# Optimization experiments

Measured on AMD Instinct MI355X. Metric: run time of the kernel, lower is better.

The kernel has to match this reference:

```python
import jax, jax.numpy as jnp
import numpy as np

NUM_GROUPS = 8
NUM_HEADS = 4
EPS = 1e-5


def group_norm(x, w, b):
    # x: [B, C, H, W]; normalize over (C/G, H, W) within each of G groups
    B, C, H, W = x.shape
    xg = x.reshape(B, NUM_GROUPS, C // NUM_GROUPS, H, W)
    mean = xg.mean(axis=(2, 3, 4), keepdims=True)
    var = xg.var(axis=(2, 3, 4), keepdims=True)
    xn = ((xg - mean) * jax.lax.rsqrt(var + EPS)).reshape(B, C, H, W)
    return xn * w[None, :, None, None] + b[None, :, None, None]


def setup_inputs() -> dict:
    key = jax.random.key(0)
    ks = jax.random.split(key, 7)
    B, C, H, W = 4, 256, 64, 64
    x = jax.random.normal(ks[0], (B, C, H, W), dtype=jnp.float32)
    gn_w = jax.random.normal(ks[1], (C,), dtype=jnp.float32) * 0.1 + 1.0
    gn_b = jax.random.normal(ks[2], (C,), dtype=jnp.float32) * 0.1
    qkv_w = jax.random.normal(ks[3], (3 * C, C), dtype=jnp.float32) / np.sqrt(C)
    qkv_b = jax.random.normal(ks[4], (3 * C,), dtype=jnp.float32) * 0.02
    proj_w = jax.random.normal(ks[5], (C, C), dtype=jnp.float32) / np.sqrt(C)
    proj_b = jax.random.normal(ks[6], (C,), dtype=jnp.float32) * 0.02
    return {"x": x, "gn_w": gn_w, "gn_b": gn_b, "qkv_w": qkv_w,
            "qkv_b": qkv_b, "proj_w": proj_w, "proj_b": proj_b}


def reference(x, gn_w, gn_b, qkv_w, qkv_b, proj_w, proj_b):
    B, C, H, W = x.shape
    nh = NUM_HEADS
    hd = C // nh
    scale = hd ** -0.5
    N = H * W

    h = group_norm(x, gn_w, gn_b)
    # 1x1 conv == channel matmul: [B, 3C, H, W]
    qkv = jnp.einsum('oc,bchw->bohw', qkv_w, h) + qkv_b[None, :, None, None]
    qkv = qkv.reshape(B, 3, nh, hd, N)  # matches torch .view(B,3,nh,hd,HW)
    q, k, v = qkv[:, 0], qkv[:, 1], qkv[:, 2]  # each [B, nh, hd, N]

    attn = jnp.einsum('bhdn,bhdm->bhnm', q, k) * scale  # [B, nh, N, N]
    attn = jax.nn.softmax(attn, axis=-1)
    out = jnp.einsum('bhnm,bhdm->bhdn', attn, v)  # [B, nh, hd, N]
    out = out.reshape(B, C, H, W)

    proj = jnp.einsum('oc,bchw->bohw', proj_w, out) + proj_b[None, :, None, None]
    return x + proj
```

## Files before the change

### kernel.cpp

```cpp
#include <hip/hip_runtime.h>
#include <hip/hip_bf16.h>

#define BB   4
#define CC   256
#define NN   4096
#define NH   4
#define HD   64
#define NG   8
#define GSZ  32
#define EPSV 1e-5f
#define SCALE_L2E 0.18033688f

typedef __bf16 bf16x8 __attribute__((ext_vector_type(8)));
typedef float  f32x4  __attribute__((ext_vector_type(4)));
typedef short  short4v __attribute__((ext_vector_type(4)));

#define MFMA16(a, b, c)  __builtin_amdgcn_mfma_f32_16x16x32_bf16((a), (b), (c), 0, 0, 0)
#define MFMAPV(a, b, c)  __builtin_amdgcn_mfma_f32_16x16x16bf16_1k((a), (b), (c), 0, 0, 0)

#if __has_builtin(__builtin_amdgcn_exp2f)
#define EXP2F __builtin_amdgcn_exp2f
#else
#define EXP2F exp2f
#endif

__device__ inline unsigned short f2bf(float f) {
    unsigned int u = __float_as_uint(f);
    u += 0x7fffu + ((u >> 16) & 1u);
    return (unsigned short)(u >> 16);
}

__device__ __forceinline__ short4v pk4(float p0, float p1, float p2, float p3) {
    alignas(8) unsigned int u[2];
    u[0] = __builtin_amdgcn_perm(__float_as_uint(p1) + 0x8000u,
                                 __float_as_uint(p0) + 0x8000u, 0x07060302u);
    u[1] = __builtin_amdgcn_perm(__float_as_uint(p3) + 0x8000u,
                                 __float_as_uint(p2) + 0x8000u, 0x07060302u);
    return *reinterpret_cast<short4v*>(u);
}

__device__ __forceinline__ void async_ld16(void* lds, const void* g) {
    __builtin_amdgcn_global_load_lds(
        (const __attribute__((address_space(1))) unsigned int*)g,
        (__attribute__((address_space(3))) unsigned int*)lds, 16, 0, 0);
}

__global__ void k_prep(const float* __restrict__ x, float* __restrict__ stats,
                       const float* __restrict__ wq, const float* __restrict__ wp,
                       unsigned short* __restrict__ oq, unsigned short* __restrict__ op) {
    int blk = blockIdx.x;
    int t = threadIdx.x;
    if (blk >= 256) {
        int i = (blk - 256) * 256 + t;
        if (i < 3 * CC * CC) oq[i] = f2bf(wq[i]);
        if (i < CC * CC)     op[i] = f2bf(wp[i]);
        return;
    }
    int b = blk >> 6, g = (blk >> 3) & 7, s = blk & 7;
    const float* p = x + ((size_t)(b * CC + g * GSZ)) * NN + s * 16384;
    float s0 = 0.f, s1 = 0.f;
    #pragma unroll
    for (int i = 0; i < 64; ++i) { float v = p[i * 256 + t]; s0 += v; s1 += v * v; }
    #pragma unroll
    for (int m = 1; m <= 32; m <<= 1) { s0 += __shfl_xor(s0, m); s1 += __shfl_xor(s1, m); }
    __shared__ float ls[8];
    int w = t >> 6;
    if ((t & 63) == 0) { ls[w * 2] = s0; ls[w * 2 + 1] = s1; }
    __syncthreads();
    if (t == 0) {
        float a0 = ls[0] + ls[2] + ls[4] + ls[6];
        float a1 = ls[1] + ls[3] + ls[5] + ls[7];
        atomicAdd(&stats[(b * NG + g) * 2 + 0], a0);
        atomicAdd(&stats[(b * NG + g) * 2 + 1], a1);
    }
}

__global__ void k_gnapply(const float* __restrict__ x, const float* __restrict__ gw,
                          const float* __restrict__ gb, const float* __restrict__ stats,
                          unsigned short* __restrict__ ht) {
    int b = blockIdx.z, ct = blockIdx.y, nt = blockIdx.x;
    int c0 = ct * 32, n0 = nt * 64;
    int t = threadIdx.x;
    __shared__ float tile[32][65];
    const float* xp = x + ((size_t)(b * CC + c0)) * NN + n0;
    int cl = t >> 6, nl = t & 63;
    #pragma unroll
    for (int p = 0; p < 8; ++p)
        tile[p * 4 + cl][nl] = xp[(size_t)(p * 4 + cl) * NN + nl];
    float sum = stats[(b * NG + ct) * 2 + 0];
    float ssq = stats[(b * NG + ct) * 2 + 1];
    float mean = sum * (1.0f / 131072.0f);
    float var  = ssq * (1.0f / 131072.0f) - mean * mean;
    float inv  = rsqrtf(var + EPSV);
    __syncthreads();
    int nw = t >> 2, ci = (t & 3) * 8;
    alignas(16) unsigned short o8[8];
    #pragma unroll
    for (int j = 0; j < 8; ++j) {
        int c = c0 + ci + j;
        float v = (tile[ci + j][nw] - mean) * inv * gw[c] + gb[c];
        o8[j] = f2bf(v);
    }
    *reinterpret_cast<uint4*>(ht + ((size_t)(b * NN + n0 + nw)) * CC + c0 + ci) =
        *reinterpret_cast<const uint4*>(o8);
}

__global__ void __launch_bounds__(256)
k_qkv(const unsigned short* __restrict__ ht, const unsigned short* __restrict__ wq,
      const float* __restrict__ qb,
      unsigned short* __restrict__ qt, unsigned short* __restrict__ kt,
      unsigned short* __restrict__ vt) {
    int bx = blockIdx.x, by = blockIdx.y;
    int t = threadIdx.x, wave = t >> 6, lane = t & 63;
    int l15 = lane & 15, quad = lane >> 4;
    int wm = wave >> 1, wn = wave & 1;

    __shared__ alignas(16) unsigned char At[2][8192];
    __shared__ alignas(16) unsigned char Bt[2][8192];

    const char* Ag = (const char*)wq + (size_t)by * 65536;
    const char* Bg = (const char*)ht + (size_t)bx * 65536;
    int row0 = t >> 2, slot = t & 3;
    size_t a0 = (size_t)row0 * 512 + slot * 16;
    size_t a1 = a0 + 64 * 512;
    unsigned int dst0 = wave * 1024;

    auto stage = [&](int buf, int kk) {
        size_t ko = (size_t)kk * 64;
        async_ld16(At[buf] + dst0,        Ag + a0 + ko);
        async_ld16(At[buf] + 4096 + dst0, Ag + a1 + ko);
        async_ld16(Bt[buf] + dst0,        Bg + a0 + ko);
        async_ld16(Bt[buf] + 4096 + dst0, Bg + a1 + ko);
    };

    f32x4 acc[4][4];
    #pragma unroll
    for (int i = 0; i < 4; ++i)
        #pragma unroll
        for (int j = 0; j < 4; ++j) acc[i][j] = (f32x4){0.f, 0.f, 0.f, 0.f};

    stage(0, 0);
    __syncthreads();

    for (int kk = 0; kk < 8; ++kk) {
        int cur = kk & 1;
        if (kk < 7) stage(cur ^ 1, kk + 1);
        bf16x8 af[4], bf[4];
        #pragma unroll
        for (int f = 0; f < 4; ++f) {
            af[f] = *reinterpret_cast<const bf16x8*>(At[cur] + (wm * 64 + f * 16 + l15) * 64 + quad * 16);
            bf[f] = *reinterpret_cast<const bf16x8*>(Bt[cur] + (wn * 64 + f * 16 + l15) * 64 + quad * 16);
        }
        #pragma unroll
        for (int fm = 0; fm < 4; ++fm)
            #pragma unroll
            for (int fn = 0; fn < 4; ++fn)
                acc[fm][fn] = MFMA16(af[fm], bf[fn], acc[fm][fn]);
        __syncthreads();
    }

    int s = by >> 1;
    int nn0 = bx * 128;
    int b = nn0 >> 12, nbase = nn0 & 4095;
    #pragma unroll
    for (int fm = 0; fm < 4; ++fm) {
        int o = by * 128 + wm * 64 + fm * 16 + quad * 4;
        int h = (o >> 6) & 3, d0 = o & 63;
        float bias[4];
        #pragma unroll
        for (int r = 0; r < 4; ++r) bias[r] = qb[o + r];
        #pragma unroll
        for (int fn = 0; fn < 4; ++fn) {
            int n = nbase + wn * 64 + fn * 16 + l15;
            if (s == 0) {
                alignas(8) unsigned short o4[4];
                #pragma unroll
                for (int r = 0; r < 4; ++r) o4[r] = f2bf((acc[fm][fn][r] + bias[r]) * SCALE_L2E);
                *reinterpret_cast<uint2*>(qt + (((size_t)(b * NH + h) * NN) + n) * HD + d0) =
                    *reinterpret_cast<const uint2*>(o4);
            } else if (s == 1) {
                alignas(8) unsigned short o4[4];
                #pragma unroll
                for (int r = 0; r < 4; ++r) o4[r] = f2bf(acc[fm][fn][r] + bias[r]);
                *reinterpret_cast<uint2*>(kt + (((size_t)(b * NH + h) * NN) + n) * HD + d0) =
                    *reinterpret_cast<const uint2*>(o4);
            } else {
                #pragma unroll
                for (int r = 0; r < 4; ++r)
                    vt[((size_t)(b * NH + h) * HD + d0 + r) * NN + n] = f2bf(acc[fm][fn][r] + bias[r]);
            }
        }
    }
}

__global__ void __launch_bounds__(256, 2)
k_attn(const unsigned short* __restrict__ qt, const unsigned short* __restrict__ kt,
       const unsigned short* __restrict__ vt, unsigned short* __restrict__ ao) {
    int bh = blockIdx.y;
    int t = threadIdx.x, wave = t >> 6, lane = t & 63;
    int l15 = lane & 15, quad = lane >> 4;
    int qbase = blockIdx.x * 128 + wave * 32;
    const unsigned short* qp = qt + (size_t)bh * NN * HD;
    const unsigned short* kp = kt + (size_t)bh * NN * HD;
    const unsigned short* vp = vt + (size_t)bh * HD * NN;

    __shared__ alignas(16) unsigned char kbuf[2][16384];
    __shared__ alignas(16) unsigned char vbuf[2][16384];

    int lr8 = lane >> 3, lc8 = lane & 7;
    const char* ksrc = (const char*)kp + (size_t)(wave * 32 + lr8) * 128 + (lc8 ^ lr8) * 16;
    int lr4 = lane >> 4, lc16 = lane & 15;
    const char* vsrc[4];
    #pragma unroll
    for (int j = 0; j < 4; ++j) {
        int rl = j * 4 + lr4;
        vsrc[j] = (const char*)vp + (size_t)(wave * 16 + rl) * 8192 + ((lc16 ^ (rl & 7)) * 16);
    }
    unsigned int dstw = wave * 4096;

    auto stage = [&](int buf) {
        #pragma unroll
        for (int j = 0; j < 4; ++j)
            async_ld16(kbuf[buf] + dstw + j * 1024, ksrc + j * 1024);
        ksrc += 16384;
        #pragma unroll
        for (int j = 0; j < 4; ++j) {
            async_ld16(vbuf[buf] + dstw + j * 1024, vsrc[j]);
            vsrc[j] += 256;
        }
    };

    bf16x8 qaA0 = *reinterpret_cast<const bf16x8*>(qp + (size_t)(qbase + l15) * HD + quad * 8);
    bf16x8 qaA1 = *reinterpret_cast<const bf16x8*>(qp + (size_t)(qbase + l15) * HD + 32 + quad * 8);
    bf16x8 qaB0 = *reinterpret_cast<const bf16x8*>(qp + (size_t)(qbase + 16 + l15) * HD + quad * 8);
    bf16x8 qaB1 = *reinterpret_cast<const bf16x8*>(qp + (size_t)(qbase + 16 + l15) * HD + 32 + quad * 8);

    f32x4 OA[4], OB[4];
    #pragma unroll
    for (int i = 0; i < 4; ++i) { OA[i] = (f32x4){0.f, 0.f, 0.f, 0.f}; OB[i] = (f32x4){0.f, 0.f, 0.f, 0.f}; }
    float liA = 0.f, liB = 0.f;

    int sx = l15 & 7;

    auto compute = [&](const unsigned char* kb, const unsigned char* vbb) {
        #pragma unroll
        for (int s = 0; s < 4; ++s) {
            int r0 = (s * 32 + l15) * 128;
            bf16x8 k00 = *reinterpret_cast<const bf16x8*>(kb + r0 + ((quad ^ sx) * 16));
            bf16x8 k01 = *reinterpret_cast<const bf16x8*>(kb + r0 + (((quad + 4) ^ sx) * 16));
            bf16x8 k10 = *reinterpret_cast<const bf16x8*>(kb + r0 + 2048 + ((quad ^ sx) * 16));
            bf16x8 k11 = *reinterpret_cast<const bf16x8*>(kb + r0 + 2048 + (((quad + 4) ^ sx) * 16));
            f32x4 sA0 = {0.f,0.f,0.f,0.f}, sA1 = {0.f,0.f,0.f,0.f};
            f32x4 sB0 = {0.f,0.f,0.f,0.f}, sB1 = {0.f,0.f,0.f,0.f};
            sA0 = MFMA16(k00, qaA0, sA0);  sA0 = MFMA16(k01, qaA1, sA0);
            sA1 = MFMA16(k10, qaA0, sA1);  sA1 = MFMA16(k11, qaA1, sA1);
            sB0 = MFMA16(k00, qaB0, sB0);  sB0 = MFMA16(k01, qaB1, sB0);
            sB1 = MFMA16(k10, qaB0, sB1);  sB1 = MFMA16(k11, qaB1, sB1);

            f32x4 pA0, pA1, pB0, pB1;
            #pragma unroll
            for (int r = 0; r < 4; ++r) {
                pA0[r] = EXP2F(sA0[r]);  pA1[r] = EXP2F(sA1[r]);
                pB0[r] = EXP2F(sB0[r]);  pB1[r] = EXP2F(sB1[r]);
            }
            liA += (pA0[0] + pA0[1] + pA0[2] + pA0[3]) + (pA1[0] + pA1[1] + pA1[2] + pA1[3]);
            liB += (pB0[0] + pB0[1] + pB0[2] + pB0[3]) + (pB1[0] + pB1[1] + pB1[2] + pB1[3]);

            short4v fA0 = pk4(pA0[0], pA0[1], pA0[2], pA0[3]);
            short4v fA1 = pk4(pA1[0], pA1[1], pA1[2], pA1[3]);
            short4v fB0 = pk4(pB0[0], pB0[1], pB0[2], pB0[3]);
            short4v fB1 = pk4(pB1[0], pB1[1], pB1[2], pB1[3]);

            #pragma unroll
            for (int dc = 0; dc < 4; ++dc) {
                int c0 = ((s * 4 + (quad >> 1)) ^ sx) * 16 + (quad & 1) * 8;
                int c1 = ((s * 4 + 2 + (quad >> 1)) ^ sx) * 16 + (quad & 1) * 8;
                const unsigned char* vrow = vbb + (dc * 16 + l15) * 256;
                short4v v0 = *reinterpret_cast<const short4v*>(vrow + c0);
                short4v v1 = *reinterpret_cast<const short4v*>(vrow + c1);
                OA[dc] = MFMAPV(fA0, v0, OA[dc]);
                OA[dc] = MFMAPV(fA1, v1, OA[dc]);
                OB[dc] = MFMAPV(fB0, v0, OB[dc]);
                OB[dc] = MFMAPV(fB1, v1, OB[dc]);
            }
        }
    };

    stage(0);
    __syncthreads();

    for (int p = 0; p < 16; ++p) {
        stage(1);
        compute(kbuf[0], vbuf[0]);
        __syncthreads();
        if (p < 15) stage(0);
        compute(kbuf[1], vbuf[1]);
        __syncthreads();
    }

    liA += __shfl_xor(liA, 16);  liA += __shfl_xor(liA, 32);
    liB += __shfl_xor(liB, 16);  liB += __shfl_xor(liB, 32);
    float invA[4], invB[4];
    #pragma unroll
    for (int r = 0; r < 4; ++r) {
        invA[r] = 1.0f / __shfl(liA, quad * 4 + r);
        invB[r] = 1.0f / __shfl(liB, quad * 4 + r);
    }

    int b = bh >> 2, h = bh & 3;
    #pragma unroll
    for (int dc = 0; dc < 4; ++dc) {
        #pragma unroll
        for (int r = 0; r < 4; ++r) {
            int qA = qbase + quad * 4 + r;
            ao[((size_t)(b * NN) + qA) * CC + h * HD + dc * 16 + l15]      = f2bf(OA[dc][r] * invA[r]);
            ao[((size_t)(b * NN) + qA + 16) * CC + h * HD + dc * 16 + l15] = f2bf(OB[dc][r] * invB[r]);
        }
    }
}

__global__ void __launch_bounds__(256)
k_proj(const unsigned short* __restrict__ ao, const unsigned short* __restrict__ wp,
       const float* __restrict__ pb, const float* __restrict__ x,
       float* __restrict__ out) {
    int bx = blockIdx.x, by = blockIdx.y;
    int t = threadIdx.x, wave = t >> 6, lane = t & 63;
    int l15 = lane & 15, quad = lane >> 4;
    int wm = wave >> 1, wn = wave & 1;

    __shared__ alignas(16) unsigned char At[2][4096];
    __shared__ alignas(16) unsigned char Bt[2][8192];

    const char* Ag = (const char*)wp + (size_t)by * 32768;
    const char* Bg = (const char*)ao + (size_t)bx * 65536;
    int row0 = t >> 2, slot = t & 3;
    size_t a0 = (size_t)row0 * 512 + slot * 16;
    size_t a1 = a0 + 64 * 512;
    unsigned int dst0 = wave * 1024;

    auto stage = [&](int buf, int kk) {
        size_t ko = (size_t)kk * 64;
        async_ld16(At[buf] + dst0,        Ag + a0 + ko);
        async_ld16(Bt[buf] + dst0,        Bg + a0 + ko);
        async_ld16(Bt[buf] + 4096 + dst0, Bg + a1 + ko);
    };

    f32x4 acc[2][4];
    #pragma unroll
    for (int i = 0; i < 2; ++i)
        #pragma unroll
        for (int j = 0; j < 4; ++j) acc[i][j] = (f32x4){0.f, 0.f, 0.f, 0.f};

    stage(0, 0);
    __syncthreads();

    for (int kk = 0; kk < 8; ++kk) {
        int cur = kk & 1;
        if (kk < 7) stage(cur ^ 1, kk + 1);
        bf16x8 af[2], bf[4];
        #pragma unroll
        for (int f = 0; f < 2; ++f)
            af[f] = *reinterpret_cast<const bf16x8*>(At[cur] + (wm * 32 + f * 16 + l15) * 64 + quad * 16);
        #pragma unroll
        for (int f = 0; f < 4; ++f)
            bf[f] = *reinterpret_cast<const bf16x8*>(Bt[cur] + (wn * 64 + f * 16 + l15) * 64 + quad * 16);
        #pragma unroll
        for (int fm = 0; fm < 2; ++fm)
            #pragma unroll
            for (int fn = 0; fn < 4; ++fn)
                acc[fm][fn] = MFMA16(af[fm], bf[fn], acc[fm][fn]);
        __syncthreads();
    }

    int nn0 = bx * 128;
    int b = nn0 >> 12, nbase = nn0 & 4095;
    #pragma unroll
    for (int fm = 0; fm < 2; ++fm) {
        int o = by * 64 + wm * 32 + fm * 16 + quad * 4;
        float bias[4];
        #pragma unroll
        for (int r = 0; r < 4; ++r) bias[r] = pb[o + r];
        #pragma unroll
        for (int fn = 0; fn < 4; ++fn) {
            int n = nbase + wn * 64 + fn * 16 + l15;
            #pragma unroll
            for (int r = 0; r < 4; ++r) {
                size_t idx = ((size_t)(b * CC + o + r)) * NN + n;
                out[idx] = acc[fm][fn][r] + bias[r] + x[idx];
            }
        }
    }
}

extern "C" void kernel_launch(void* const* d_in, const int* in_sizes, int n_in,
                              void* d_out, int out_size, void* d_ws, size_t ws_size,
                              hipStream_t stream) {
    const float* x     = (const float*)d_in[0];
    const float* gw    = (const float*)d_in[1];
    const float* gb    = (const float*)d_in[2];
    const float* qkvw  = (const float*)d_in[3];
    const float* qkvb  = (const float*)d_in[4];
    const float* projw = (const float*)d_in[5];
    const float* projb = (const float*)d_in[6];
    float* out = (float*)d_out;

    char* w = (char*)d_ws;
    size_t off = 0;
    unsigned short* ht = (unsigned short*)(w + off); off += (size_t)BB * NN * CC * 2;
    unsigned short* qt = (unsigned short*)(w + off); off += (size_t)BB * NH * NN * HD * 2;
    unsigned short* kt = (unsigned short*)(w + off); off += (size_t)BB * NH * NN * HD * 2;
    unsigned short* vt = (unsigned short*)(w + off); off += (size_t)BB * NH * HD * NN * 2;
    unsigned short* ao = (unsigned short*)(w + off); off += (size_t)BB * NN * CC * 2;
    unsigned short* wqb = (unsigned short*)(w + off); off += (size_t)3 * CC * CC * 2;
    unsigned short* wpb = (unsigned short*)(w + off); off += (size_t)CC * CC * 2;
    float* stats = (float*)(w + off); off += BB * NG * 2 * sizeof(float);

    hipMemsetAsync(stats, 0, BB * NG * 2 * sizeof(float), stream);
    k_prep<<<1024, 256, 0, stream>>>(x, stats, qkvw, projw, wqb, wpb);
    k_gnapply<<<dim3(NN / 64, CC / 32, BB), 256, 0, stream>>>(x, gw, gb, stats, ht);
    k_qkv<<<dim3(BB * NN / 128, 6), 256, 0, stream>>>(ht, wqb, qkvb, qt, kt, vt);
    k_attn<<<dim3(NN / 128, BB * NH), 256, 0, stream>>>(qt, kt, vt, ao);
    k_proj<<<dim3(BB * NN / 128, CC / 64), 256, 0, stream>>>(ao, wpb, projb, x, out);
}
```

Baseline: 200.9 us.

## Split attention over key halves with combine kernel and smaller proj tiles

```diff
diff --git a/kernel.cpp b/kernel.cpp
--- a/kernel.cpp
+++ b/kernel.cpp
@@ -30,12 +30,10 @@
     return (unsigned short)(u >> 16);
 }
 
-__device__ __forceinline__ short4v pk4(float p0, float p1, float p2, float p3) {
+__device__ __forceinline__ short4v pk4(const f32x4& p) {
     alignas(8) unsigned int u[2];
-    u[0] = __builtin_amdgcn_perm(__float_as_uint(p1) + 0x8000u,
-                                 __float_as_uint(p0) + 0x8000u, 0x07060302u);
-    u[1] = __builtin_amdgcn_perm(__float_as_uint(p3) + 0x8000u,
-                                 __float_as_uint(p2) + 0x8000u, 0x07060302u);
+    u[0] = __builtin_amdgcn_perm(__float_as_uint(p[1]), __float_as_uint(p[0]), 0x07060302u);
+    u[1] = __builtin_amdgcn_perm(__float_as_uint(p[3]), __float_as_uint(p[2]), 0x07060302u);
     return *reinterpret_cast<short4v*>(u);
 }
 
@@ -193,41 +191,37 @@
     }
 }
 
-__global__ void __launch_bounds__(256, 2)
+__global__ void __launch_bounds__(256, 4)
 k_attn(const unsigned short* __restrict__ qt, const unsigned short* __restrict__ kt,
-       const unsigned short* __restrict__ vt, unsigned short* __restrict__ ao) {
+       const unsigned short* __restrict__ vt,
+       unsigned short* __restrict__ op0, unsigned short* __restrict__ op1,
+       float* __restrict__ lip) {
     int bh = blockIdx.y;
+    int split = blockIdx.z;
     int t = threadIdx.x, wave = t >> 6, lane = t & 63;
     int l15 = lane & 15, quad = lane >> 4;
     int qbase = blockIdx.x * 128 + wave * 32;
+    int kbase = split * 2048;
     const unsigned short* qp = qt + (size_t)bh * NN * HD;
     const unsigned short* kp = kt + (size_t)bh * NN * HD;
     const unsigned short* vp = vt + (size_t)bh * HD * NN;
 
-    __shared__ alignas(16) unsigned char kbuf[2][16384];
-    __shared__ alignas(16) unsigned char vbuf[2][16384];
+    __shared__ alignas(16) unsigned char kbuf[2][8192];
+    __shared__ alignas(16) unsigned char vbuf[2][8192];
 
     int lr8 = lane >> 3, lc8 = lane & 7;
-    const char* ksrc = (const char*)kp + (size_t)(wave * 32 + lr8) * 128 + (lc8 ^ lr8) * 16;
-    int lr4 = lane >> 4, lc16 = lane & 15;
-    const char* vsrc[4];
-    #pragma unroll
-    for (int j = 0; j < 4; ++j) {
-        int rl = j * 4 + lr4;
-        vsrc[j] = (const char*)vp + (size_t)(wave * 16 + rl) * 8192 + ((lc16 ^ (rl & 7)) * 16);
-    }
-    unsigned int dstw = wave * 4096;
+    int swz = lc8 ^ lr8;
+    const char* ksrc = (const char*)kp + (size_t)(kbase + wave * 16 + lr8) * 128 + swz * 16;
+    const char* vsrc = (const char*)vp + (size_t)(wave * 16 + lr8) * 8192 + (size_t)kbase * 2 + swz * 16;
+    unsigned int dstw = wave * 2048;
 
     auto stage = [&](int buf) {
-        #pragma unroll
-        for (int j = 0; j < 4; ++j)
-            async_ld16(kbuf[buf] + dstw + j * 1024, ksrc + j * 1024);
-        ksrc += 16384;
-        #pragma unroll
-        for (int j = 0; j < 4; ++j) {
-            async_ld16(vbuf[buf] + dstw + j * 1024, vsrc[j]);
-            vsrc[j] += 256;
-        }
+        async_ld16(kbuf[buf] + dstw,        ksrc);
+        async_ld16(kbuf[buf] + dstw + 1024, ksrc + 1024);
+        ksrc += 8192;
+        async_ld16(vbuf[buf] + dstw,        vsrc);
+        async_ld16(vbuf[buf] + dstw + 1024, vsrc + 8 * 8192);
+        vsrc += 128;
     };
 
     bf16x8 qaA0 = *reinterpret_cast<const bf16x8*>(qp + (size_t)(qbase + l15) * HD + quad * 8);
@@ -244,7 +238,7 @@
 
     auto compute = [&](const unsigned char* kb, const unsigned char* vbb) {
         #pragma unroll
-        for (int s = 0; s < 4; ++s) {
+        for (int s = 0; s < 2; ++s) {
             int r0 = (s * 32 + l15) * 128;
             bf16x8 k00 = *reinterpret_cast<const bf16x8*>(kb + r0 + ((quad ^ sx) * 16));
             bf16x8 k01 = *reinterpret_cast<const bf16x8*>(kb + r0 + (((quad + 4) ^ sx) * 16));
@@ -266,16 +260,13 @@
             liA += (pA0[0] + pA0[1] + pA0[2] + pA0[3]) + (pA1[0] + pA1[1] + pA1[2] + pA1[3]);
             liB += (pB0[0] + pB0[1] + pB0[2] + pB0[3]) + (pB1[0] + pB1[1] + pB1[2] + pB1[3]);
 
-            short4v fA0 = pk4(pA0[0], pA0[1], pA0[2], pA0[3]);
-            short4v fA1 = pk4(pA1[0], pA1[1], pA1[2], pA1[3]);
-            short4v fB0 = pk4(pB0[0], pB0[1], pB0[2], pB0[3]);
-            short4v fB1 = pk4(pB1[0], pB1[1], pB1[2], pB1[3]);
+            short4v fA0 = pk4(pA0), fA1 = pk4(pA1), fB0 = pk4(pB0), fB1 = pk4(pB1);
 
             #pragma unroll
             for (int dc = 0; dc < 4; ++dc) {
                 int c0 = ((s * 4 + (quad >> 1)) ^ sx) * 16 + (quad & 1) * 8;
                 int c1 = ((s * 4 + 2 + (quad >> 1)) ^ sx) * 16 + (quad & 1) * 8;
-                const unsigned char* vrow = vbb + (dc * 16 + l15) * 256;
+                const unsigned char* vrow = vbb + (dc * 16 + l15) * 128;
                 short4v v0 = *reinterpret_cast<const short4v*>(vrow + c0);
                 short4v v1 = *reinterpret_cast<const short4v*>(vrow + c1);
                 OA[dc] = MFMAPV(fA0, v0, OA[dc]);
@@ -300,23 +291,47 @@
 
     liA += __shfl_xor(liA, 16);  liA += __shfl_xor(liA, 32);
     liB += __shfl_xor(liB, 16);  liB += __shfl_xor(liB, 32);
-    float invA[4], invB[4];
-    #pragma unroll
-    for (int r = 0; r < 4; ++r) {
-        invA[r] = 1.0f / __shfl(liA, quad * 4 + r);
-        invB[r] = 1.0f / __shfl(liB, quad * 4 + r);
-    }
-
+
+    unsigned short* op = split ? op1 : op0;
     int b = bh >> 2, h = bh & 3;
     #pragma unroll
     for (int dc = 0; dc < 4; ++dc) {
         #pragma unroll
         for (int r = 0; r < 4; ++r) {
             int qA = qbase + quad * 4 + r;
-            ao[((size_t)(b * NN) + qA) * CC + h * HD + dc * 16 + l15]      = f2bf(OA[dc][r] * invA[r]);
-            ao[((size_t)(b * NN) + qA + 16) * CC + h * HD + dc * 16 + l15] = f2bf(OB[dc][r] * invB[r]);
-        }
-    }
+            op[((size_t)(b * NN) + qA) * CC + h * HD + dc * 16 + l15]      = f2bf(OA[dc][r]);
+            op[((size_t)(b * NN) + qA + 16) * CC + h * HD + dc * 16 + l15] = f2bf(OB[dc][r]);
+        }
+    }
+    float* lp = lip + (size_t)split * (16 * NN) + (size_t)bh * NN + qbase;
+    if (quad == 0)      lp[l15]      = liA;
+    else if (quad == 1) lp[16 + l15] = liB;
+}
+
+__global__ void __launch_bounds__(256)
+k_comb(unsigned short* ao, const unsigned short* __restrict__ p1, const float* __restrict__ lip) {
+    int g = blockIdx.x * 256 + threadIdx.x;
+    int d8 = g & 7;
+    int h  = (g >> 3) & 3;
+    int n  = (g >> 5) & 4095;
+    int b  = g >> 17;
+    int bh = b * 4 + h;
+    float li0 = lip[(size_t)bh * NN + n];
+    float li1 = lip[(size_t)16 * NN + (size_t)bh * NN + n];
+    float inv = 1.0f / (li0 + li1);
+    size_t idx = ((size_t)(b * NN) + n) * CC + h * HD + d8 * 8;
+    uint4 u0 = *reinterpret_cast<const uint4*>(ao + idx);
+    uint4 u1 = *reinterpret_cast<const uint4*>(p1 + idx);
+    const unsigned short* a0 = reinterpret_cast<const unsigned short*>(&u0);
+    const unsigned short* a1 = reinterpret_cast<const unsigned short*>(&u1);
+    alignas(16) unsigned short o8[8];
+    #pragma unroll
+    for (int i = 0; i < 8; ++i) {
+        float f0 = __uint_as_float((unsigned)a0[i] << 16);
+        float f1 = __uint_as_float((unsigned)a1[i] << 16);
+        o8[i] = f2bf((f0 + f1) * inv);
+    }
+    *reinterpret_cast<uint4*>(ao + idx) = *reinterpret_cast<const uint4*>(o8);
 }
 
 __global__ void __launch_bounds__(256)
@@ -329,27 +344,25 @@
     int wm = wave >> 1, wn = wave & 1;
 
     __shared__ alignas(16) unsigned char At[2][4096];
-    __shared__ alignas(16) unsigned char Bt[2][8192];
+    __shared__ alignas(16) unsigned char Bt[2][4096];
 
     const char* Ag = (const char*)wp + (size_t)by * 32768;
-    const char* Bg = (const char*)ao + (size_t)bx * 65536;
+    const char* Bg = (const char*)ao + (size_t)bx * 32768;
     int row0 = t >> 2, slot = t & 3;
     size_t a0 = (size_t)row0 * 512 + slot * 16;
-    size_t a1 = a0 + 64 * 512;
     unsigned int dst0 = wave * 1024;
 
     auto stage = [&](int buf, int kk) {
         size_t ko = (size_t)kk * 64;
-        async_ld16(At[buf] + dst0,        Ag + a0 + ko);
-        async_ld16(Bt[buf] + dst0,        Bg + a0 + ko);
-        async_ld16(Bt[buf] + 4096 + dst0, Bg + a1 + ko);
+        async_ld16(At[buf] + dst0, Ag + a0 + ko);
+        async_ld16(Bt[buf] + dst0, Bg + a0 + ko);
     };
 
-    f32x4 acc[2][4];
+    f32x4 acc[2][2];
     #pragma unroll
     for (int i = 0; i < 2; ++i)
         #pragma unroll
-        for (int j = 0; j < 4; ++j) acc[i][j] = (f32x4){0.f, 0.f, 0.f, 0.f};
+        for (int j = 0; j < 2; ++j) acc[i][j] = (f32x4){0.f, 0.f, 0.f, 0.f};
 
     stage(0, 0);
     __syncthreads();
@@ -357,22 +370,21 @@
     for (int kk = 0; kk < 8; ++kk) {
         int cur = kk & 1;
         if (kk < 7) stage(cur ^ 1, kk + 1);
-        bf16x8 af[2], bf[4];
-        #pragma unroll
-        for (int f = 0; f < 2; ++f)
+        bf16x8 af[2], bf[2];
+        #pragma unroll
+        for (int f = 0; f < 2; ++f) {
             af[f] = *reinterpret_cast<const bf16x8*>(At[cur] + (wm * 32 + f * 16 + l15) * 64 + quad * 16);
-        #pragma unroll
-        for (int f = 0; f < 4; ++f)
-            bf[f] = *reinterpret_cast<const bf16x8*>(Bt[cur] + (wn * 64 + f * 16 + l15) * 64 + quad * 16);
+            bf[f] = *reinterpret_cast<const bf16x8*>(Bt[cur] + (wn * 32 + f * 16 + l15) * 64 + quad * 16);
+        }
         #pragma unroll
         for (int fm = 0; fm < 2; ++fm)
             #pragma unroll
-            for (int fn = 0; fn < 4; ++fn)
+            for (int fn = 0; fn < 2; ++fn)
                 acc[fm][fn] = MFMA16(af[fm], bf[fn], acc[fm][fn]);
         __syncthreads();
     }
 
-    int nn0 = bx * 128;
+    int nn0 = bx * 64;
     int b = nn0 >> 12, nbase = nn0 & 4095;
     #pragma unroll
     for (int fm = 0; fm < 2; ++fm) {
@@ -381,8 +393,8 @@
         #pragma unroll
         for (int r = 0; r < 4; ++r) bias[r] = pb[o + r];
         #pragma unroll
-        for (int fn = 0; fn < 4; ++fn) {
-            int n = nbase + wn * 64 + fn * 16 + l15;
+        for (int fn = 0; fn < 2; ++fn) {
+            int n = nbase + wn * 32 + fn * 16 + l15;
             #pragma unroll
             for (int r = 0; r < 4; ++r) {
                 size_t idx = ((size_t)(b * CC + o + r)) * NN + n;
@@ -414,11 +426,13 @@
     unsigned short* wqb = (unsigned short*)(w + off); off += (size_t)3 * CC * CC * 2;
     unsigned short* wpb = (unsigned short*)(w + off); off += (size_t)CC * CC * 2;
     float* stats = (float*)(w + off); off += BB * NG * 2 * sizeof(float);
+    float* lip   = (float*)(w + off); off += (size_t)2 * 16 * NN * sizeof(float);
 
     hipMemsetAsync(stats, 0, BB * NG * 2 * sizeof(float), stream);
     k_prep<<<1024, 256, 0, stream>>>(x, stats, qkvw, projw, wqb, wpb);
     k_gnapply<<<dim3(NN / 64, CC / 32, BB), 256, 0, stream>>>(x, gw, gb, stats, ht);
     k_qkv<<<dim3(BB * NN / 128, 6), 256, 0, stream>>>(ht, wqb, qkvb, qt, kt, vt);
-    k_attn<<<dim3(NN / 128, BB * NH), 256, 0, stream>>>(qt, kt, vt, ao);
-    k_proj<<<dim3(BB * NN / 128, CC / 64), 256, 0, stream>>>(ao, wpb, projb, x, out);
-}
+    k_attn<<<dim3(NN / 128, BB * NH, 2), 256, 0, stream>>>(qt, kt, vt, ao, ht, lip);
+    k_comb<<<2048, 256, 0, stream>>>(ao, ht, lip);
+    k_proj<<<dim3(BB * NN / 64, CC / 64), 256, 0, stream>>>(ao, wpb, projb, x, out);
+}
```

Measured after the change: 199.2 us. Within noise of the previous version (-0.8%).
